# Performance work log

Hardware: AMD Instinct MI355X
Metric: run time of the kernel (lower is better)

The kernel has to match this reference:

```python
import jax, jax.numpy as jnp
import numpy as np

DIM = 1024
HEADS = 16
HEAD_DIM = DIM // HEADS
B, N = 4, 4096


def setup_inputs() -> dict:
    key = jax.random.key(0)
    ks = jax.random.split(key, 10)
    s = 1.0 / np.sqrt(DIM)
    return {
        "x": jax.random.normal(ks[0], (B, N, DIM), dtype=jnp.float32),
        "Wq": jax.random.uniform(ks[1], (DIM, DIM), jnp.float32, -s, s),
        "bq": jax.random.uniform(ks[2], (DIM,), jnp.float32, -s, s),
        "Wk": jax.random.uniform(ks[3], (DIM, DIM), jnp.float32, -s, s),
        "bk": jax.random.uniform(ks[4], (DIM,), jnp.float32, -s, s),
        "Wv": jax.random.uniform(ks[5], (DIM, DIM), jnp.float32, -s, s),
        "bv": jax.random.uniform(ks[6], (DIM,), jnp.float32, -s, s),
        "Wo": jax.random.uniform(ks[7], (DIM, DIM), jnp.float32, -s, s),
        "bo": jax.random.uniform(ks[8], (DIM,), jnp.float32, -s, s),
        "stdp": jnp.ones((HEADS,), dtype=jnp.float32),
    }


def reference(x, Wq, bq, Wk, bk, Wv, bv, Wo, bo, stdp):
    b, n, d = x.shape
    h, dh = HEADS, HEAD_DIM
    # projections (torch Linear: x @ W.T + b)
    def proj(W, bias):
        return (x @ W.T + bias).reshape(b, n, h, dh).transpose(0, 2, 1, 3)  # bhnd
    Q = jax.nn.elu(proj(Wq, bq)) + 1.0
    K = jax.nn.elu(proj(Wk, bk)) + 1.0
    V = proj(Wv, bv)
    stdp_w = jax.nn.sigmoid(stdp).reshape(1, h, 1, 1)
    KV = jnp.einsum('bhnd,bhnv->bhdv', K, V)      # (b,h,dh,dh)
    K_sum = K.sum(axis=2)                          # (b,h,dh)
    numerator = jnp.einsum('bhnd,bhdv->bhnv', Q, KV)
    denominator = jnp.einsum('bhnd,bhd->bhn', Q, K_sum)[..., None] + 1e-6
    attn_out = numerator / denominator * stdp_w    # (b,h,n,dh)
    out = attn_out.transpose(0, 2, 1, 3).reshape(b, n, d)
    out = out @ Wo.T + bo
    return (out, jax.lax.stop_gradient(stdp))
```

## Files before the change

### kernel.cpp

```cpp
#include <hip/hip_runtime.h>
#include <hip/hip_bf16.h>

#define DIMSZ 1024
#define SEQLEN 4096
#define NHEAD 16
#define NX 16777216L
#define NW 1048576L
#define KVSPLITS 8

typedef __attribute__((ext_vector_type(8))) short bf16x8;
typedef __attribute__((ext_vector_type(4))) float f32x4;

__device__ __forceinline__ unsigned short f2bf(float f) {
    union { float f; unsigned int i; } c; c.f = f;
    unsigned int x = c.i;
    unsigned int r = (x + 0x7fffu + ((x >> 16) & 1u)) >> 16;
    return (unsigned short)r;
}

__device__ __forceinline__ unsigned int pk2(float lo, float hi) {
    union { float f; unsigned int i; } a, b; a.f = lo; b.f = hi;
    return __builtin_amdgcn_perm(b.i + 0x8000u, a.i + 0x8000u, 0x07060302u);
}

__device__ __forceinline__ void unp8r(bf16x8 v, float* f) {
    union { bf16x8 s; uint4 w; } u; u.s = v;
    union { unsigned int i; float f; } c;
    c.i = u.w.x << 16;           f[0] = c.f;
    c.i = u.w.x & 0xffff0000u;   f[1] = c.f;
    c.i = u.w.y << 16;           f[2] = c.f;
    c.i = u.w.y & 0xffff0000u;   f[3] = c.f;
    c.i = u.w.z << 16;           f[4] = c.f;
    c.i = u.w.z & 0xffff0000u;   f[5] = c.f;
    c.i = u.w.w << 16;           f[6] = c.f;
    c.i = u.w.w & 0xffff0000u;   f[7] = c.f;
}

__device__ __forceinline__ void async16(const void* g, void* l) {
    __builtin_amdgcn_global_load_lds(
        (const __attribute__((address_space(1))) void*)g,
        (__attribute__((address_space(3))) void*)l,
        16, 0, 0);
}

__global__ __launch_bounds__(256) void cast_pack(
    const float* __restrict__ x, const float* __restrict__ Wq,
    const float* __restrict__ Wk, const float* __restrict__ Wv,
    const float* __restrict__ Wo, const float* __restrict__ stdp,
    unsigned short* __restrict__ xb, unsigned short* __restrict__ Wqkv,
    unsigned short* __restrict__ Wob, float* __restrict__ outTail)
{
    long i4 = ((long)blockIdx.x * 256 + threadIdx.x) * 4;
    const float* src; unsigned short* dst; long off;
    if (i4 < NX)               { src = x;  dst = xb;          off = i4; }
    else if (i4 < NX + NW)     { src = Wq; dst = Wqkv;        off = i4 - NX; }
    else if (i4 < NX + 2*NW)   { src = Wk; dst = Wqkv + NW;   off = i4 - NX - NW; }
    else if (i4 < NX + 3*NW)   { src = Wv; dst = Wqkv + 2*NW; off = i4 - NX - 2*NW; }
    else                       { src = Wo; dst = Wob;         off = i4 - NX - 3*NW; }
    float4 v = *(const float4*)(src + off);
    union { unsigned short u[4]; uint2 p; } o;
    o.u[0] = f2bf(v.x); o.u[1] = f2bf(v.y); o.u[2] = f2bf(v.z); o.u[3] = f2bf(v.w);
    *(uint2*)(dst + off) = o.p;
    if (blockIdx.x == 0 && threadIdx.x < NHEAD) outTail[threadIdx.x] = stdp[threadIdx.x];
}

__global__ __launch_bounds__(512, 2) void qkv_gemm8(
    const unsigned short* __restrict__ A, const unsigned short* __restrict__ W,
    const float* __restrict__ bq, const float* __restrict__ bk,
    const float* __restrict__ bv,
    unsigned short* __restrict__ Qb, unsigned short* __restrict__ Kb,
    unsigned short* __restrict__ Vb)
{
    __shared__ __align__(16) char SM[131072];
    const int t = threadIdx.x;
    const int wave = t >> 6, lane = t & 63;
    const int lr = lane & 15, lq = lane >> 4;
    const int wm = wave >> 2, wn = wave & 3;
    const int m0 = blockIdx.x * 256;
    const int c0 = blockIdx.y * 256;

    const int sc = (((t & 7) ^ ((t >> 3) & 7)) * 8);
    const unsigned short* pA = A + (long)(m0 + (t >> 3)) * DIMSZ + sc;
    const unsigned short* pB = W + (long)(c0 + (t >> 3)) * DIMSZ + sc;
    char* ldsW = SM + wave * 1024;

    const int xo = ((lq ^ (lr & 7)) << 4);
    const char* ABase = SM + wm * 16384 + lr * 128;
    const char* BBase = SM + 32768 + (wn * 64 + lr) * 128;

    f32x4 acc[8][4];
    #pragma unroll
    for (int i = 0; i < 8; ++i)
        #pragma unroll
        for (int j = 0; j < 4; ++j) acc[i][j] = (f32x4){0.f, 0.f, 0.f, 0.f};

#define STAGE(Q, O) do {                                                        \
        if ((Q) < 16) {                                                         \
            const int isB_ = ((O) < 2) ? 1 : 0;                                 \
            const int half_ = isB_ ? (O) : ((O) - 2);                           \
            const unsigned short* s_ = (isB_ ? pB : pA)                         \
                                       + (long)half_ * 131072 + (Q) * 64;       \
            char* d_ = ldsW + (((Q) & 1) << 16) + isB_ * 32768 + half_ * 16384; \
            async16(s_, d_);                                                    \
            async16(s_ + 65536, d_ + 8192);                                     \
        }                                                                       \
    } while (0)

    STAGE(0, 0); STAGE(0, 1); STAGE(0, 2); STAGE(0, 3);
    STAGE(1, 0); STAGE(1, 1); STAGE(1, 2);
    asm volatile("s_waitcnt vmcnt(6)" ::: "memory");
    __builtin_amdgcn_s_barrier();

    for (int kt = 0; kt < 16; ++kt) {
        const int buf = (kt & 1) << 16;
        bf16x8 a0[4][2], a1[4][2], bfr[4][2];

        #pragma unroll
        for (int j = 0; j < 2; ++j) {
            bfr[j][0] = *(const bf16x8*)(BBase + buf + j * 2048 + xo);
            bfr[j][1] = *(const bf16x8*)(BBase + buf + j * 2048 + (xo ^ 64));
        }
        #pragma unroll
        for (int i = 0; i < 4; ++i) {
            a0[i][0] = *(const bf16x8*)(ABase + buf + i * 2048 + xo);
            a0[i][1] = *(const bf16x8*)(ABase + buf + i * 2048 + (xo ^ 64));
        }
        __builtin_amdgcn_sched_barrier(0);
        #pragma unroll
        for (int j = 2; j < 4; ++j) {
            bfr[j][0] = *(const bf16x8*)(BBase + buf + j * 2048 + xo);
            bfr[j][1] = *(const bf16x8*)(BBase + buf + j * 2048 + (xo ^ 64));
        }
        __builtin_amdgcn_sched_barrier(0);
        #pragma unroll
        for (int i = 0; i < 4; ++i) {
            a1[i][0] = *(const bf16x8*)(ABase + buf + (i + 4) * 2048 + xo);
            a1[i][1] = *(const bf16x8*)(ABase + buf + (i + 4) * 2048 + (xo ^ 64));
        }
        __builtin_amdgcn_sched_barrier(0);
        STAGE(kt + 1, 3);

        asm volatile("s_waitcnt lgkmcnt(12)" ::: "memory");
        __builtin_amdgcn_sched_barrier(0);
        __builtin_amdgcn_s_setprio(1);
        #pragma unroll
        for (int s = 0; s < 2; ++s)
            #pragma unroll
            for (int i = 0; i < 4; ++i)
                #pragma unroll
                for (int j = 0; j < 2; ++j)
                    acc[i][j] = __builtin_amdgcn_mfma_f32_16x16x32_bf16(
                        bfr[j][s], a0[i][s], acc[i][j], 0, 0, 0);
        __builtin_amdgcn_s_setprio(0);

        asm volatile("s_waitcnt lgkmcnt(8)" ::: "memory");
        __builtin_amdgcn_sched_barrier(0);
        __builtin_amdgcn_s_setprio(1);
        #pragma unroll
        for (int s = 0; s < 2; ++s)
            #pragma unroll
            for (int i = 0; i < 4; ++i)
                #pragma unroll
                for (int j = 2; j < 4; ++j)
                    acc[i][j] = __builtin_amdgcn_mfma_f32_16x16x32_bf16(
                        bfr[j][s], a0[i][s], acc[i][j], 0, 0, 0);
        __builtin_amdgcn_s_setprio(0);

        asm volatile("s_waitcnt lgkmcnt(0)" ::: "memory");
        __builtin_amdgcn_sched_barrier(0);
        __builtin_amdgcn_s_setprio(1);
        #pragma unroll
        for (int s = 0; s < 2; ++s)
            #pragma unroll
            for (int i = 0; i < 4; ++i)
                #pragma unroll
                for (int j = 0; j < 2; ++j)
                    acc[i + 4][j] = __builtin_amdgcn_mfma_f32_16x16x32_bf16(
                        bfr[j][s], a1[i][s], acc[i + 4][j], 0, 0, 0);
        __builtin_amdgcn_s_setprio(0);

        __builtin_amdgcn_s_barrier();
        STAGE(kt + 2, 0); STAGE(kt + 2, 1); STAGE(kt + 2, 2);

        __builtin_amdgcn_s_setprio(1);
        #pragma unroll
        for (int s = 0; s < 2; ++s)
            #pragma unroll
            for (int i = 0; i < 4; ++i)
                #pragma unroll
                for (int j = 2; j < 4; ++j)
                    acc[i + 4][j] = __builtin_amdgcn_mfma_f32_16x16x32_bf16(
                        bfr[j][s], a1[i][s], acc[i + 4][j], 0, 0, 0);
        __builtin_amdgcn_s_setprio(0);

        if (kt < 14)       asm volatile("s_waitcnt vmcnt(6)" ::: "memory");
        else if (kt == 14) asm volatile("s_waitcnt vmcnt(0)" ::: "memory");
        __builtin_amdgcn_s_barrier();
    }
#undef STAGE

    const int proj = c0 >> 10;
    const float* bias = proj == 0 ? bq : (proj == 1 ? bk : bv);
    const bool qk = proj < 2;
    const int cb = (c0 & 1023) + wn * 64;
    const int q4 = lq * 4;
    #pragma unroll
    for (int j = 0; j < 4; ++j) {
        const float4 b4 = *(const float4*)(bias + cb + 16 * j + q4);
        #pragma unroll
        for (int i = 0; i < 8; ++i) {
            float v0 = acc[i][j][0] + b4.x, v1 = acc[i][j][1] + b4.y;
            float v2 = acc[i][j][2] + b4.z, v3 = acc[i][j][3] + b4.w;
            if (qk) {
                v0 = v0 > 0.f ? v0 + 1.f : __expf(v0);
                v1 = v1 > 0.f ? v1 + 1.f : __expf(v1);
                v2 = v2 > 0.f ? v2 + 1.f : __expf(v2);
                v3 = v3 > 0.f ? v3 + 1.f : __expf(v3);
            }
            const int row = wm * 128 + 16 * i + lr;
            int byte = row * 512 + wn * 128 + j * 32 + q4 * 2;
            byte ^= (row & 7) << 4;
            uint2 pkd; pkd.x = pk2(v0, v1); pkd.y = pk2(v2, v3);
            *(uint2*)(SM + byte) = pkd;
        }
    }
    __syncthreads();
    unsigned short* dstp = proj == 0 ? Qb : (proj == 1 ? Kb : Vb);
    const int colsh = (t & 31) * 8;
    const int h = ((c0 >> 6) + (colsh >> 6)) & 15;
    const int b_ = m0 >> 12;
    unsigned short* dbase = dstp + ((long)(b_ * 16 + h) * SEQLEN) * 64 + (colsh & 63);
    #pragma unroll
    for (int u = 0; u < 16; ++u) {
        const int flat = u * 8192 + t * 16;
        const int row = flat >> 9;
        uint4 val = *(const uint4*)(SM + (flat ^ ((row & 7) << 4)));
        const int n = (m0 + row) & 4095;
        *(uint4*)(dbase + (long)n * 64) = val;
    }
}

__global__ __launch_bounds__(256) void kv_reduce(
    const unsigned short* __restrict__ Kb, const unsigned short* __restrict__ Vb,
    float* __restrict__ KVp, float* __restrict__ Ksump)
{
    __shared__ __align__(16) char LDS[65536];
    int bh = blockIdx.x, split = blockIdx.y, t = threadIdx.x;
    int wave = t >> 6, lane = t & 63, lr = lane & 15, lq = lane >> 4;

    const int nl = t & 127;
    const int dh = (t >> 7) * 32;
    const int vrow = 16 * wave + lr;

    f32x4 acc[4];
    #pragma unroll
    for (int j = 0; j < 4; ++j) acc[j] = (f32x4){0.f, 0.f, 0.f, 0.f};
    float ksp[4] = {0.f, 0.f, 0.f, 0.f};

    for (int half = 0; half < 2; ++half) {
        const unsigned short* Kbase = Kb + ((long)bh * SEQLEN + split * 512 + half * 256) * 64;
        const unsigned short* Vbase = Vb + ((long)bh * SEQLEN + split * 512 + half * 256) * 64;

        union Q2S { uint4 q[4]; unsigned short s[32]; };
        Q2S kq[2], vq[2];
        #pragma unroll
        for (int it = 0; it < 2; ++it) {
            const unsigned short* kp = Kbase + (long)(it * 128 + nl) * 64 + dh;
            const unsigned short* vp = Vbase + (long)(it * 128 + nl) * 64 + dh;
            #pragma unroll
            for (int g = 0; g < 4; ++g) {
                kq[it].q[g] = *(const uint4*)(kp + g * 8);
                vq[it].q[g] = *(const uint4*)(vp + g * 8);
            }
        }
        if (half) __syncthreads();
        #pragma unroll
        for (int it = 0; it < 2; ++it) {
            char* buf = LDS + it * 32768;
            #pragma unroll
            for (int e = 0; e < 32; ++e) {
                const int d = dh + e;
                const int a = d * 256 + ((nl * 2) ^ ((d & 7) << 4));
                *(unsigned short*)(buf + a) = kq[it].s[e];
                *(unsigned short*)(buf + 16384 + a) = vq[it].s[e];
            }
        }
        __syncthreads();

        #pragma unroll
        for (int it = 0; it < 2; ++it) {
            const char* buf = LDS + it * 32768;
            #pragma unroll
            for (int ns = 0; ns < 4; ++ns) {
                const int xoff = (ns * 64 + lq * 16) ^ ((lr & 7) << 4);
                bf16x8 af = *(const bf16x8*)(buf + 16384 + vrow * 256 + xoff);
                bf16x8 bfr[4];
                #pragma unroll
                for (int j = 0; j < 4; ++j)
                    bfr[j] = *(const bf16x8*)(buf + (16 * j + lr) * 256 + xoff);
                if (wave == 0) {
                    #pragma unroll
                    for (int j = 0; j < 4; ++j) {
                        float kf[8]; unp8r(bfr[j], kf);
                        ksp[j] += ((kf[0] + kf[1]) + (kf[2] + kf[3]))
                                + ((kf[4] + kf[5]) + (kf[6] + kf[7]));
                    }
                }
                #pragma unroll
                for (int j = 0; j < 4; ++j)
                    acc[j] = __builtin_amdgcn_mfma_f32_16x16x32_bf16(bfr[j], af, acc[j], 0, 0, 0);
            }
        }
    }

    float* kp = KVp + ((long)split * 64 + bh) * 4096;
    const int q4 = lq * 4;
    #pragma unroll
    for (int j = 0; j < 4; ++j)
        *(f32x4*)(kp + vrow * 64 + 16 * j + q4) = acc[j];

    if (wave == 0) {
        #pragma unroll
        for (int j = 0; j < 4; ++j) {
            float s = ksp[j];
            s += __shfl_xor(s, 16);
            s += __shfl_xor(s, 32);
            if (lane < 16)
                Ksump[((long)split * 64 + bh) * 64 + 16 * j + lr] = s;
        }
    }
}

__global__ __launch_bounds__(256) void kv_final(
    const float* __restrict__ KVp, const float* __restrict__ Ksump,
    unsigned short* __restrict__ KVb, float* __restrict__ Ksum)
{
    int bh = blockIdx.x, t = threadIdx.x;
    float s[16];
    #pragma unroll
    for (int g = 0; g < 16; ++g) s[g] = 0.f;
    for (int sp = 0; sp < KVSPLITS; ++sp) {
        const float* src = KVp + ((long)sp * 64 + bh) * 4096 + t * 16;
        #pragma unroll
        for (int g = 0; g < 4; ++g) {
            float4 v = *(const float4*)(src + g * 4);
            s[g * 4 + 0] += v.x; s[g * 4 + 1] += v.y;
            s[g * 4 + 2] += v.z; s[g * 4 + 3] += v.w;
        }
    }
    uint4 o0, o1;
    o0.x = pk2(s[0], s[1]);  o0.y = pk2(s[2], s[3]);
    o0.z = pk2(s[4], s[5]);  o0.w = pk2(s[6], s[7]);
    o1.x = pk2(s[8], s[9]);  o1.y = pk2(s[10], s[11]);
    o1.z = pk2(s[12], s[13]); o1.w = pk2(s[14], s[15]);
    *(uint4*)(KVb + (long)bh * 4096 + t * 16) = o0;
    *(uint4*)(KVb + (long)bh * 4096 + t * 16 + 8) = o1;
    if (t < 16) {
        float4 a = {0.f, 0.f, 0.f, 0.f};
        for (int p = 0; p < KVSPLITS; p += 4) {
            #pragma unroll
            for (int q = 0; q < 4; ++q) {
                float4 v = *(const float4*)(Ksump + ((long)(p + q) * 64 + bh) * 64 + t * 4);
                a.x += v.x; a.y += v.y; a.z += v.z; a.w += v.w;
            }
        }
        *(float4*)(Ksum + bh * 64 + t * 4) = a;
    }
}

__global__ __launch_bounds__(256) void attn_kernel(
    const unsigned short* __restrict__ Qb, const unsigned short* __restrict__ KVb,
    const float* __restrict__ Ksum, const float* __restrict__ stdp,
    unsigned short* __restrict__ attn)
{
    __shared__ unsigned short Cs[256 * 72];
    int t = threadIdx.x;
    int bh = blockIdx.y;
    int b = bh >> 4, h = bh & 15;

    int wave = t >> 6, lane = t & 63, lr = lane & 15, lk = (lane >> 4) * 8;
    const unsigned short* kvb = KVb + (long)bh * 4096;
    const float* ksb = Ksum + bh * 64;

    bf16x8 bfrh[2][4];
    float ksf[2][8];
    #pragma unroll
    for (int s = 0; s < 2; ++s) {
        #pragma unroll
        for (int j = 0; j < 4; ++j)
            bfrh[s][j] = *(const bf16x8*)(kvb + (16 * j + lr) * 64 + s * 32 + lk);
        float4 ka = *(const float4*)(ksb + s * 32 + lk);
        float4 kb2 = *(const float4*)(ksb + s * 32 + lk + 4);
        ksf[s][0] = ka.x; ksf[s][1] = ka.y; ksf[s][2] = ka.z; ksf[s][3] = ka.w;
        ksf[s][4] = kb2.x; ksf[s][5] = kb2.y; ksf[s][6] = kb2.z; ksf[s][7] = kb2.w;
    }
    float sg = 1.f / (1.f + __expf(-stdp[h]));
    int q4 = (lane >> 4) * 4;

    for (int c = 0; c < 2; ++c) {
        int rc = blockIdx.x * 2 + c;
        int rowbase = rc * 256 + wave * 64;

        f32x4 acc[4][4];
        #pragma unroll
        for (int i = 0; i < 4; ++i)
            #pragma unroll
            for (int j = 0; j < 4; ++j) acc[i][j] = (f32x4){0.f, 0.f, 0.f, 0.f};
        float ds[4] = {0.f, 0.f, 0.f, 0.f};

        #pragma unroll
        for (int s = 0; s < 2; ++s) {
            bf16x8 af[4];
            #pragma unroll
            for (int i = 0; i < 4; ++i)
                af[i] = *(const bf16x8*)(Qb + ((long)bh * SEQLEN + rowbase + 16 * i + lr) * 64 + s * 32 + lk);
            #pragma unroll
            for (int i = 0; i < 4; ++i) {
                float qf[8]; unp8r(af[i], qf);
                #pragma unroll
                for (int e = 0; e < 8; ++e) ds[i] += qf[e] * ksf[s][e];
            }
            #pragma unroll
            for (int i = 0; i < 4; ++i)
                #pragma unroll
                for (int j = 0; j < 4; ++j)
                    acc[i][j] = __builtin_amdgcn_mfma_f32_16x16x32_bf16(bfrh[s][j], af[i], acc[i][j], 0, 0, 0);
        }

        float dinv_i[4];
        #pragma unroll
        for (int i = 0; i < 4; ++i) {
            float d = ds[i];
            d += __shfl_xor(d, 16);
            d += __shfl_xor(d, 32);
            dinv_i[i] = sg / (d + 1e-6f);
        }

        #pragma unroll
        for (int j = 0; j < 4; ++j) {
            int v0c = 16 * j + q4;
            #pragma unroll
            for (int i = 0; i < 4; ++i) {
                int row = wave * 64 + 16 * i + lr;
                float d = dinv_i[i];
                uint2 pkd;
                pkd.x = pk2(acc[i][j][0] * d, acc[i][j][1] * d);
                pkd.y = pk2(acc[i][j][2] * d, acc[i][j][3] * d);
                *(uint2*)(Cs + row * 72 + v0c) = pkd;
            }
        }
        __syncthreads();
        #pragma unroll
        for (int u = 0; u < 8; ++u) {
            int row = u * 32 + (t >> 3);
            int nn = rc * 256 + row;
            long a = ((long)(b * SEQLEN + nn)) * DIMSZ + h * 64 + (t & 7) * 8;
            *(uint4*)(attn + a) = *(const uint4*)(Cs + row * 72 + (t & 7) * 8);
        }
        __syncthreads();
    }
}

__global__ __launch_bounds__(512, 2) void out_gemm8(
    const unsigned short* __restrict__ A, const unsigned short* __restrict__ W,
    const float* __restrict__ bo, float* __restrict__ out)
{
    __shared__ __align__(16) char SM[131072];
    const int t = threadIdx.x;
    const int wave = t >> 6, lane = t & 63;
    const int lr = lane & 15, lq = lane >> 4;
    const int wm = wave >> 2, wn = wave & 3;
    const int m0 = blockIdx.x * 256;
    const int c0 = blockIdx.y * 256;

    const int sc = (((t & 7) ^ ((t >> 3) & 7)) * 8);
    const unsigned short* pA = A + (long)(m0 + (t >> 3)) * DIMSZ + sc;
    const unsigned short* pB = W + (long)(c0 + (t >> 3)) * DIMSZ + sc;
    char* ldsW = SM + wave * 1024;

    const int xo = ((lq ^ (lr & 7)) << 4);
    const char* ABase = SM + wm * 16384 + lr * 128;
    const char* BBase = SM + 32768 + (wn * 64 + lr) * 128;

    f32x4 acc[8][4];
    #pragma unroll
    for (int i = 0; i < 8; ++i)
        #pragma unroll
        for (int j = 0; j < 4; ++j) acc[i][j] = (f32x4){0.f, 0.f, 0.f, 0.f};

#define STAGE(Q, O) do {                                                        \
        if ((Q) < 16) {                                                         \
            const int isB_ = ((O) < 2) ? 1 : 0;                                 \
            const int half_ = isB_ ? (O) : ((O) - 2);                           \
            const unsigned short* s_ = (isB_ ? pB : pA)                         \
                                       + (long)half_ * 131072 + (Q) * 64;       \
            char* d_ = ldsW + (((Q) & 1) << 16) + isB_ * 32768 + half_ * 16384; \
            async16(s_, d_);                                                    \
            async16(s_ + 65536, d_ + 8192);                                     \
        }                                                                       \
    } while (0)

    STAGE(0, 0); STAGE(0, 1); STAGE(0, 2); STAGE(0, 3);
    STAGE(1, 0); STAGE(1, 1); STAGE(1, 2);
    asm volatile("s_waitcnt vmcnt(6)" ::: "memory");
    __builtin_amdgcn_s_barrier();

    for (int kt = 0; kt < 16; ++kt) {
        const int buf = (kt & 1) << 16;
        bf16x8 a0[4][2], a1[4][2], bfr[4][2];

        #pragma unroll
        for (int j = 0; j < 2; ++j) {
            bfr[j][0] = *(const bf16x8*)(BBase + buf + j * 2048 + xo);
            bfr[j][1] = *(const bf16x8*)(BBase + buf + j * 2048 + (xo ^ 64));
        }
        #pragma unroll
        for (int i = 0; i < 4; ++i) {
            a0[i][0] = *(const bf16x8*)(ABase + buf + i * 2048 + xo);
            a0[i][1] = *(const bf16x8*)(ABase + buf + i * 2048 + (xo ^ 64));
        }
        __builtin_amdgcn_sched_barrier(0);
        #pragma unroll
        for (int j = 2; j < 4; ++j) {
            bfr[j][0] = *(const bf16x8*)(BBase + buf + j * 2048 + xo);
            bfr[j][1] = *(const bf16x8*)(BBase + buf + j * 2048 + (xo ^ 64));
        }
        __builtin_amdgcn_sched_barrier(0);
        #pragma unroll
        for (int i = 0; i < 4; ++i) {
            a1[i][0] = *(const bf16x8*)(ABase + buf + (i + 4) * 2048 + xo);
            a1[i][1] = *(const bf16x8*)(ABase + buf + (i + 4) * 2048 + (xo ^ 64));
        }
        __builtin_amdgcn_sched_barrier(0);
        STAGE(kt + 1, 3);

        asm volatile("s_waitcnt lgkmcnt(12)" ::: "memory");
        __builtin_amdgcn_sched_barrier(0);
        __builtin_amdgcn_s_setprio(1);
        #pragma unroll
        for (int s = 0; s < 2; ++s)
            #pragma unroll
            for (int i = 0; i < 4; ++i)
                #pragma unroll
                for (int j = 0; j < 2; ++j)
                    acc[i][j] = __builtin_amdgcn_mfma_f32_16x16x32_bf16(
                        bfr[j][s], a0[i][s], acc[i][j], 0, 0, 0);
        __builtin_amdgcn_s_setprio(0);

        asm volatile("s_waitcnt lgkmcnt(8)" ::: "memory");
        __builtin_amdgcn_sched_barrier(0);
        __builtin_amdgcn_s_setprio(1);
        #pragma unroll
        for (int s = 0; s < 2; ++s)
            #pragma unroll
            for (int i = 0; i < 4; ++i)
                #pragma unroll
                for (int j = 2; j < 4; ++j)
                    acc[i][j] = __builtin_amdgcn_mfma_f32_16x16x32_bf16(
                        bfr[j][s], a0[i][s], acc[i][j], 0, 0, 0);
        __builtin_amdgcn_s_setprio(0);

        asm volatile("s_waitcnt lgkmcnt(0)" ::: "memory");
        __builtin_amdgcn_sched_barrier(0);
        __builtin_amdgcn_s_setprio(1);
        #pragma unroll
        for (int s = 0; s < 2; ++s)
            #pragma unroll
            for (int i = 0; i < 4; ++i)
                #pragma unroll
                for (int j = 0; j < 2; ++j)
                    acc[i + 4][j] = __builtin_amdgcn_mfma_f32_16x16x32_bf16(
                        bfr[j][s], a1[i][s], acc[i + 4][j], 0, 0, 0);
        __builtin_amdgcn_s_setprio(0);

        __builtin_amdgcn_s_barrier();
        STAGE(kt + 2, 0); STAGE(kt + 2, 1); STAGE(kt + 2, 2);

        __builtin_amdgcn_s_setprio(1);
        #pragma unroll
        for (int s = 0; s < 2; ++s)
            #pragma unroll
            for (int i = 0; i < 4; ++i)
                #pragma unroll
                for (int j = 2; j < 4; ++j)
                    acc[i + 4][j] = __builtin_amdgcn_mfma_f32_16x16x32_bf16(
                        bfr[j][s], a1[i][s], acc[i + 4][j], 0, 0, 0);
        __builtin_amdgcn_s_setprio(0);

        if (kt < 14)       asm volatile("s_waitcnt vmcnt(6)" ::: "memory");
        else if (kt == 14) asm volatile("s_waitcnt vmcnt(0)" ::: "memory");
        __builtin_amdgcn_s_barrier();
    }
#undef STAGE

    const int q4 = lq * 4;
    #pragma unroll
    for (int j = 0; j < 4; ++j) {
        const int c = c0 + wn * 64 + 16 * j + q4;
        const float4 b4 = *(const float4*)(bo + c);
        #pragma unroll
        for (int i = 0; i < 8; ++i) {
            const int gm = m0 + wm * 128 + 16 * i + lr;
            float4 v;
            v.x = acc[i][j][0] + b4.x; v.y = acc[i][j][1] + b4.y;
            v.z = acc[i][j][2] + b4.z; v.w = acc[i][j][3] + b4.w;
            *(float4*)(out + (long)gm * DIMSZ + c) = v;
        }
    }
}

extern "C" void kernel_launch(void* const* d_in, const int* in_sizes, int n_in,
                              void* d_out, int out_size, void* d_ws, size_t ws_size,
                              hipStream_t stream) {
    const float* x    = (const float*)d_in[0];
    const float* Wq   = (const float*)d_in[1];
    const float* bq   = (const float*)d_in[2];
    const float* Wk   = (const float*)d_in[3];
    const float* bk   = (const float*)d_in[4];
    const float* Wv   = (const float*)d_in[5];
    const float* bv   = (const float*)d_in[6];
    const float* Wo   = (const float*)d_in[7];
    const float* bo   = (const float*)d_in[8];
    const float* stdp = (const float*)d_in[9];
    float* out = (float*)d_out;

    char* ws = (char*)d_ws;
    unsigned short* xb   = (unsigned short*)(ws);
    float*          KVp  = (float*)(ws);
    unsigned short* attn = (unsigned short*)(ws);
    unsigned short* Wqkv = (unsigned short*)(ws + 33554432L);
    float*          Ksump= (float*)(ws + 33554432L);
    unsigned short* KVb  = (unsigned short*)(ws + 33816576L);
    float*          Ksum = (float*)(ws + 34340864L);
    unsigned short* Wob  = (unsigned short*)(ws + 39845888L);
    unsigned short* Qb   = (unsigned short*)(ws + 41943040L);
    unsigned short* Kb   = (unsigned short*)(ws + 75497472L);
    unsigned short* Vb   = (unsigned short*)(ws + 109051904L);

    cast_pack<<<20480, 256, 0, stream>>>(x, Wq, Wk, Wv, Wo, stdp, xb, Wqkv, Wob,
                                         out + 16777216L);
    qkv_gemm8<<<dim3(64, 12), 512, 0, stream>>>(xb, Wqkv, bq, bk, bv, Qb, Kb, Vb);
    kv_reduce<<<dim3(64, KVSPLITS), 256, 0, stream>>>(Kb, Vb, KVp, Ksump);
    kv_final<<<64, 256, 0, stream>>>(KVp, Ksump, KVb, Ksum);
    attn_kernel<<<dim3(8, 64), 256, 0, stream>>>(Qb, KVb, Ksum, stdp, attn);
    out_gemm8<<<dim3(64, 4), 512, 0, stream>>>(attn, Wob, bo, out);
}
```

Measured before the change: 315.4 us.

## Use 1024-thread blocks in GEMMs with 16 waves sharing each 256x256 tile

Both bf16 GEMM kernels go from 512 threads (8 waves, 128x64 per wave) to 1024 threads (16 waves, 64x64 per wave) on the same 256x256 block tile. Each thread issues half the async global-to-LDS copies, and the K-slice of fragment loads is split into two halves to cut register pressure. The goal is more waves to hide memory latency and fewer accumulators per thread. The cost is one block per CU, since the launch bounds change from (512,2) to (1024,1) with 128KB of LDS per block, plus more barrier participants and less fragment reuse per wave.

```diff
diff --git a/kernel.cpp b/kernel.cpp
--- a/kernel.cpp
+++ b/kernel.cpp
@@ -64,7 +64,7 @@
     if (blockIdx.x == 0 && threadIdx.x < NHEAD) outTail[threadIdx.x] = stdp[threadIdx.x];
 }
 
-__global__ __launch_bounds__(512, 2) void qkv_gemm8(
+__global__ __launch_bounds__(1024, 1) void qkv_gemm8(
     const unsigned short* __restrict__ A, const unsigned short* __restrict__ W,
     const float* __restrict__ bq, const float* __restrict__ bk,
     const float* __restrict__ bv,
@@ -85,12 +85,12 @@
     char* ldsW = SM + wave * 1024;
 
     const int xo = ((lq ^ (lr & 7)) << 4);
-    const char* ABase = SM + wm * 16384 + lr * 128;
+    const char* ABase = SM + wm * 8192 + lr * 128;
     const char* BBase = SM + 32768 + (wn * 64 + lr) * 128;
 
-    f32x4 acc[8][4];
-    #pragma unroll
-    for (int i = 0; i < 8; ++i)
+    f32x4 acc[4][4];
+    #pragma unroll
+    for (int i = 0; i < 4; ++i)
         #pragma unroll
         for (int j = 0; j < 4; ++j) acc[i][j] = (f32x4){0.f, 0.f, 0.f, 0.f};
 
@@ -102,98 +102,87 @@
                                        + (long)half_ * 131072 + (Q) * 64;       \
             char* d_ = ldsW + (((Q) & 1) << 16) + isB_ * 32768 + half_ * 16384; \
             async16(s_, d_);                                                    \
-            async16(s_ + 65536, d_ + 8192);                                     \
         }                                                                       \
     } while (0)
 
     STAGE(0, 0); STAGE(0, 1); STAGE(0, 2); STAGE(0, 3);
     STAGE(1, 0); STAGE(1, 1); STAGE(1, 2);
-    asm volatile("s_waitcnt vmcnt(6)" ::: "memory");
+    asm volatile("s_waitcnt vmcnt(3)" ::: "memory");
     __builtin_amdgcn_s_barrier();
 
     for (int kt = 0; kt < 16; ++kt) {
         const int buf = (kt & 1) << 16;
-        bf16x8 a0[4][2], a1[4][2], bfr[4][2];
-
-        #pragma unroll
-        for (int j = 0; j < 2; ++j) {
-            bfr[j][0] = *(const bf16x8*)(BBase + buf + j * 2048 + xo);
-            bfr[j][1] = *(const bf16x8*)(BBase + buf + j * 2048 + (xo ^ 64));
-        }
-        #pragma unroll
-        for (int i = 0; i < 4; ++i) {
-            a0[i][0] = *(const bf16x8*)(ABase + buf + i * 2048 + xo);
-            a0[i][1] = *(const bf16x8*)(ABase + buf + i * 2048 + (xo ^ 64));
-        }
-        __builtin_amdgcn_sched_barrier(0);
-        #pragma unroll
-        for (int j = 2; j < 4; ++j) {
-            bfr[j][0] = *(const bf16x8*)(BBase + buf + j * 2048 + xo);
-            bfr[j][1] = *(const bf16x8*)(BBase + buf + j * 2048 + (xo ^ 64));
-        }
-        __builtin_amdgcn_sched_barrier(0);
-        #pragma unroll
-        for (int i = 0; i < 4; ++i) {
-            a1[i][0] = *(const bf16x8*)(ABase + buf + (i + 4) * 2048 + xo);
-            a1[i][1] = *(const bf16x8*)(ABase + buf + (i + 4) * 2048 + (xo ^ 64));
-        }
+        bf16x8 a[4], b[4];
+
+        b[0] = *(const bf16x8*)(BBase + buf + 0 * 2048 + xo);
+        b[1] = *(const bf16x8*)(BBase + buf + 1 * 2048 + xo);
+        #pragma unroll
+        for (int i = 0; i < 4; ++i)
+            a[i] = *(const bf16x8*)(ABase + buf + i * 2048 + xo);
+        __builtin_amdgcn_sched_barrier(0);
+        b[2] = *(const bf16x8*)(BBase + buf + 2 * 2048 + xo);
+        b[3] = *(const bf16x8*)(BBase + buf + 3 * 2048 + xo);
         __builtin_amdgcn_sched_barrier(0);
         STAGE(kt + 1, 3);
 
-        asm volatile("s_waitcnt lgkmcnt(12)" ::: "memory");
-        __builtin_amdgcn_sched_barrier(0);
-        __builtin_amdgcn_s_setprio(1);
-        #pragma unroll
-        for (int s = 0; s < 2; ++s)
-            #pragma unroll
-            for (int i = 0; i < 4; ++i)
-                #pragma unroll
-                for (int j = 0; j < 2; ++j)
-                    acc[i][j] = __builtin_amdgcn_mfma_f32_16x16x32_bf16(
-                        bfr[j][s], a0[i][s], acc[i][j], 0, 0, 0);
-        __builtin_amdgcn_s_setprio(0);
-
-        asm volatile("s_waitcnt lgkmcnt(8)" ::: "memory");
-        __builtin_amdgcn_sched_barrier(0);
-        __builtin_amdgcn_s_setprio(1);
-        #pragma unroll
-        for (int s = 0; s < 2; ++s)
-            #pragma unroll
-            for (int i = 0; i < 4; ++i)
-                #pragma unroll
-                for (int j = 2; j < 4; ++j)
-                    acc[i][j] = __builtin_amdgcn_mfma_f32_16x16x32_bf16(
-                        bfr[j][s], a0[i][s], acc[i][j], 0, 0, 0);
+        asm volatile("s_waitcnt lgkmcnt(2)" ::: "memory");
+        __builtin_amdgcn_sched_barrier(0);
+        __builtin_amdgcn_s_setprio(1);
+        #pragma unroll
+        for (int i = 0; i < 4; ++i)
+            #pragma unroll
+            for (int j = 0; j < 2; ++j)
+                acc[i][j] = __builtin_amdgcn_mfma_f32_16x16x32_bf16(
+                    b[j], a[i], acc[i][j], 0, 0, 0);
         __builtin_amdgcn_s_setprio(0);
 
         asm volatile("s_waitcnt lgkmcnt(0)" ::: "memory");
         __builtin_amdgcn_sched_barrier(0);
         __builtin_amdgcn_s_setprio(1);
         #pragma unroll
-        for (int s = 0; s < 2; ++s)
-            #pragma unroll
-            for (int i = 0; i < 4; ++i)
-                #pragma unroll
-                for (int j = 0; j < 2; ++j)
-                    acc[i + 4][j] = __builtin_amdgcn_mfma_f32_16x16x32_bf16(
-                        bfr[j][s], a1[i][s], acc[i + 4][j], 0, 0, 0);
-        __builtin_amdgcn_s_setprio(0);
-
+        for (int i = 0; i < 4; ++i)
+            #pragma unroll
+            for (int j = 2; j < 4; ++j)
+                acc[i][j] = __builtin_amdgcn_mfma_f32_16x16x32_bf16(
+                    b[j], a[i], acc[i][j], 0, 0, 0);
+        __builtin_amdgcn_s_setprio(0);
+
+        b[0] = *(const bf16x8*)(BBase + buf + 0 * 2048 + (xo ^ 64));
+        b[1] = *(const bf16x8*)(BBase + buf + 1 * 2048 + (xo ^ 64));
+        #pragma unroll
+        for (int i = 0; i < 4; ++i)
+            a[i] = *(const bf16x8*)(ABase + buf + i * 2048 + (xo ^ 64));
+        __builtin_amdgcn_sched_barrier(0);
+        b[2] = *(const bf16x8*)(BBase + buf + 2 * 2048 + (xo ^ 64));
+        b[3] = *(const bf16x8*)(BBase + buf + 3 * 2048 + (xo ^ 64));
+        __builtin_amdgcn_sched_barrier(0);
+
+        asm volatile("s_waitcnt lgkmcnt(2)" ::: "memory");
+        __builtin_amdgcn_sched_barrier(0);
+        __builtin_amdgcn_s_setprio(1);
+        #pragma unroll
+        for (int i = 0; i < 4; ++i)
+            #pragma unroll
+            for (int j = 0; j < 2; ++j)
+                acc[i][j] = __builtin_amdgcn_mfma_f32_16x16x32_bf16(
+                    b[j], a[i], acc[i][j], 0, 0, 0);
+        __builtin_amdgcn_s_setprio(0);
+
+        asm volatile("s_waitcnt lgkmcnt(0)" ::: "memory");
+        __builtin_amdgcn_sched_barrier(0);
         __builtin_amdgcn_s_barrier();
         STAGE(kt + 2, 0); STAGE(kt + 2, 1); STAGE(kt + 2, 2);
 
         __builtin_amdgcn_s_setprio(1);
         #pragma unroll
-        for (int s = 0; s < 2; ++s)
-            #pragma unroll
-            for (int i = 0; i < 4; ++i)
-                #pragma unroll
-                for (int j = 2; j < 4; ++j)
-                    acc[i + 4][j] = __builtin_amdgcn_mfma_f32_16x16x32_bf16(
-                        bfr[j][s], a1[i][s], acc[i + 4][j], 0, 0, 0);
-        __builtin_amdgcn_s_setprio(0);
-
-        if (kt < 14)       asm volatile("s_waitcnt vmcnt(6)" ::: "memory");
+        for (int i = 0; i < 4; ++i)
+            #pragma unroll
+            for (int j = 2; j < 4; ++j)
+                acc[i][j] = __builtin_amdgcn_mfma_f32_16x16x32_bf16(
+                    b[j], a[i], acc[i][j], 0, 0, 0);
+        __builtin_amdgcn_s_setprio(0);
+
+        if (kt < 14)       asm volatile("s_waitcnt vmcnt(3)" ::: "memory");
         else if (kt == 14) asm volatile("s_waitcnt vmcnt(0)" ::: "memory");
         __builtin_amdgcn_s_barrier();
     }
@@ -208,7 +197,7 @@
     for (int j = 0; j < 4; ++j) {
         const float4 b4 = *(const float4*)(bias + cb + 16 * j + q4);
         #pragma unroll
-        for (int i = 0; i < 8; ++i) {
+        for (int i = 0; i < 4; ++i) {
             float v0 = acc[i][j][0] + b4.x, v1 = acc[i][j][1] + b4.y;
             float v2 = acc[i][j][2] + b4.z, v3 = acc[i][j][3] + b4.w;
             if (qk) {
@@ -217,7 +206,7 @@
                 v2 = v2 > 0.f ? v2 + 1.f : __expf(v2);
                 v3 = v3 > 0.f ? v3 + 1.f : __expf(v3);
             }
-            const int row = wm * 128 + 16 * i + lr;
+            const int row = wm * 64 + 16 * i + lr;
             int byte = row * 512 + wn * 128 + j * 32 + q4 * 2;
             byte ^= (row & 7) << 4;
             uint2 pkd; pkd.x = pk2(v0, v1); pkd.y = pk2(v2, v3);
@@ -231,8 +220,8 @@
     const int b_ = m0 >> 12;
     unsigned short* dbase = dstp + ((long)(b_ * 16 + h) * SEQLEN) * 64 + (colsh & 63);
     #pragma unroll
-    for (int u = 0; u < 16; ++u) {
-        const int flat = u * 8192 + t * 16;
+    for (int u = 0; u < 8; ++u) {
+        const int flat = u * 16384 + t * 16;
         const int row = flat >> 9;
         uint4 val = *(const uint4*)(SM + (flat ^ ((row & 7) << 4)));
         const int n = (m0 + row) & 4095;
@@ -461,7 +450,7 @@
     }
 }
 
-__global__ __launch_bounds__(512, 2) void out_gemm8(
+__global__ __launch_bounds__(1024, 1) void out_gemm8(
     const unsigned short* __restrict__ A, const unsigned short* __restrict__ W,
     const float* __restrict__ bo, float* __restrict__ out)
 {
@@ -479,12 +468,12 @@
     char* ldsW = SM + wave * 1024;
 
     const int xo = ((lq ^ (lr & 7)) << 4);
-    const char* ABase = SM + wm * 16384 + lr * 128;
+    const char* ABase = SM + wm * 8192 + lr * 128;
     const char* BBase = SM + 32768 + (wn * 64 + lr) * 128;
 
-    f32x4 acc[8][4];
-    #pragma unroll
-    for (int i = 0; i < 8; ++i)
+    f32x4 acc[4][4];
+    #pragma unroll
+    for (int i = 0; i < 4; ++i)
         #pragma unroll
         for (int j = 0; j < 4; ++j) acc[i][j] = (f32x4){0.f, 0.f, 0.f, 0.f};
 
@@ -496,98 +485,87 @@
                                        + (long)half_ * 131072 + (Q) * 64;       \
             char* d_ = ldsW + (((Q) & 1) << 16) + isB_ * 32768 + half_ * 16384; \
             async16(s_, d_);                                                    \
-            async16(s_ + 65536, d_ + 8192);                                     \
         }                                                                       \
     } while (0)
 
     STAGE(0, 0); STAGE(0, 1); STAGE(0, 2); STAGE(0, 3);
     STAGE(1, 0); STAGE(1, 1); STAGE(1, 2);
-    asm volatile("s_waitcnt vmcnt(6)" ::: "memory");
+    asm volatile("s_waitcnt vmcnt(3)" ::: "memory");
     __builtin_amdgcn_s_barrier();
 
     for (int kt = 0; kt < 16; ++kt) {
         const int buf = (kt & 1) << 16;
-        bf16x8 a0[4][2], a1[4][2], bfr[4][2];
-
-        #pragma unroll
-        for (int j = 0; j < 2; ++j) {
-            bfr[j][0] = *(const bf16x8*)(BBase + buf + j * 2048 + xo);
-            bfr[j][1] = *(const bf16x8*)(BBase + buf + j * 2048 + (xo ^ 64));
-        }
-        #pragma unroll
-        for (int i = 0; i < 4; ++i) {
-            a0[i][0] = *(const bf16x8*)(ABase + buf + i * 2048 + xo);
-            a0[i][1] = *(const bf16x8*)(ABase + buf + i * 2048 + (xo ^ 64));
-        }
-        __builtin_amdgcn_sched_barrier(0);
-        #pragma unroll
-        for (int j = 2; j < 4; ++j) {
-            bfr[j][0] = *(const bf16x8*)(BBase + buf + j * 2048 + xo);
-            bfr[j][1] = *(const bf16x8*)(BBase + buf + j * 2048 + (xo ^ 64));
-        }
-        __builtin_amdgcn_sched_barrier(0);
-        #pragma unroll
-        for (int i = 0; i < 4; ++i) {
-            a1[i][0] = *(const bf16x8*)(ABase + buf + (i + 4) * 2048 + xo);
-            a1[i][1] = *(const bf16x8*)(ABase + buf + (i + 4) * 2048 + (xo ^ 64));
-        }
+        bf16x8 a[4], b[4];
+
+        b[0] = *(const bf16x8*)(BBase + buf + 0 * 2048 + xo);
+        b[1] = *(const bf16x8*)(BBase + buf + 1 * 2048 + xo);
+        #pragma unroll
+        for (int i = 0; i < 4; ++i)
+            a[i] = *(const bf16x8*)(ABase + buf + i * 2048 + xo);
+        __builtin_amdgcn_sched_barrier(0);
+        b[2] = *(const bf16x8*)(BBase + buf + 2 * 2048 + xo);
+        b[3] = *(const bf16x8*)(BBase + buf + 3 * 2048 + xo);
         __builtin_amdgcn_sched_barrier(0);
         STAGE(kt + 1, 3);
 
-        asm volatile("s_waitcnt lgkmcnt(12)" ::: "memory");
-        __builtin_amdgcn_sched_barrier(0);
-        __builtin_amdgcn_s_setprio(1);
-        #pragma unroll
-        for (int s = 0; s < 2; ++s)
-            #pragma unroll
-            for (int i = 0; i < 4; ++i)
-                #pragma unroll
-                for (int j = 0; j < 2; ++j)
-                    acc[i][j] = __builtin_amdgcn_mfma_f32_16x16x32_bf16(
-                        bfr[j][s], a0[i][s], acc[i][j], 0, 0, 0);
-        __builtin_amdgcn_s_setprio(0);
-
-        asm volatile("s_waitcnt lgkmcnt(8)" ::: "memory");
-        __builtin_amdgcn_sched_barrier(0);
-        __builtin_amdgcn_s_setprio(1);
-        #pragma unroll
-        for (int s = 0; s < 2; ++s)
-            #pragma unroll
-            for (int i = 0; i < 4; ++i)
-                #pragma unroll
-                for (int j = 2; j < 4; ++j)
-                    acc[i][j] = __builtin_amdgcn_mfma_f32_16x16x32_bf16(
-                        bfr[j][s], a0[i][s], acc[i][j], 0, 0, 0);
+        asm volatile("s_waitcnt lgkmcnt(2)" ::: "memory");
+        __builtin_amdgcn_sched_barrier(0);
+        __builtin_amdgcn_s_setprio(1);
+        #pragma unroll
+        for (int i = 0; i < 4; ++i)
+            #pragma unroll
+            for (int j = 0; j < 2; ++j)
+                acc[i][j] = __builtin_amdgcn_mfma_f32_16x16x32_bf16(
+                    b[j], a[i], acc[i][j], 0, 0, 0);
         __builtin_amdgcn_s_setprio(0);
 
         asm volatile("s_waitcnt lgkmcnt(0)" ::: "memory");
         __builtin_amdgcn_sched_barrier(0);
         __builtin_amdgcn_s_setprio(1);
         #pragma unroll
-        for (int s = 0; s < 2; ++s)
-            #pragma unroll
-            for (int i = 0; i < 4; ++i)
-                #pragma unroll
-                for (int j = 0; j < 2; ++j)
-                    acc[i + 4][j] = __builtin_amdgcn_mfma_f32_16x16x32_bf16(
-                        bfr[j][s], a1[i][s], acc[i + 4][j], 0, 0, 0);
-        __builtin_amdgcn_s_setprio(0);
-
+        for (int i = 0; i < 4; ++i)
+            #pragma unroll
+            for (int j = 2; j < 4; ++j)
+                acc[i][j] = __builtin_amdgcn_mfma_f32_16x16x32_bf16(
+                    b[j], a[i], acc[i][j], 0, 0, 0);
+        __builtin_amdgcn_s_setprio(0);
+
+        b[0] = *(const bf16x8*)(BBase + buf + 0 * 2048 + (xo ^ 64));
+        b[1] = *(const bf16x8*)(BBase + buf + 1 * 2048 + (xo ^ 64));
+        #pragma unroll
+        for (int i = 0; i < 4; ++i)
+            a[i] = *(const bf16x8*)(ABase + buf + i * 2048 + (xo ^ 64));
+        __builtin_amdgcn_sched_barrier(0);
+        b[2] = *(const bf16x8*)(BBase + buf + 2 * 2048 + (xo ^ 64));
+        b[3] = *(const bf16x8*)(BBase + buf + 3 * 2048 + (xo ^ 64));
+        __builtin_amdgcn_sched_barrier(0);
+
+        asm volatile("s_waitcnt lgkmcnt(2)" ::: "memory");
+        __builtin_amdgcn_sched_barrier(0);
+        __builtin_amdgcn_s_setprio(1);
+        #pragma unroll
+        for (int i = 0; i < 4; ++i)
+            #pragma unroll
+            for (int j = 0; j < 2; ++j)
+                acc[i][j] = __builtin_amdgcn_mfma_f32_16x16x32_bf16(
+                    b[j], a[i], acc[i][j], 0, 0, 0);
+        __builtin_amdgcn_s_setprio(0);
+
+        asm volatile("s_waitcnt lgkmcnt(0)" ::: "memory");
+        __builtin_amdgcn_sched_barrier(0);
         __builtin_amdgcn_s_barrier();
         STAGE(kt + 2, 0); STAGE(kt + 2, 1); STAGE(kt + 2, 2);
 
         __builtin_amdgcn_s_setprio(1);
         #pragma unroll
-        for (int s = 0; s < 2; ++s)
-            #pragma unroll
-            for (int i = 0; i < 4; ++i)
-                #pragma unroll
-                for (int j = 2; j < 4; ++j)
-                    acc[i + 4][j] = __builtin_amdgcn_mfma_f32_16x16x32_bf16(
-                        bfr[j][s], a1[i][s], acc[i + 4][j], 0, 0, 0);
-        __builtin_amdgcn_s_setprio(0);
-
-        if (kt < 14)       asm volatile("s_waitcnt vmcnt(6)" ::: "memory");
+        for (int i = 0; i < 4; ++i)
+            #pragma unroll
+            for (int j = 2; j < 4; ++j)
+                acc[i][j] = __builtin_amdgcn_mfma_f32_16x16x32_bf16(
+                    b[j], a[i], acc[i][j], 0, 0, 0);
+        __builtin_amdgcn_s_setprio(0);
+
+        if (kt < 14)       asm volatile("s_waitcnt vmcnt(3)" ::: "memory");
         else if (kt == 14) asm volatile("s_waitcnt vmcnt(0)" ::: "memory");
         __builtin_amdgcn_s_barrier();
     }
@@ -599,8 +577,8 @@
         const int c = c0 + wn * 64 + 16 * j + q4;
         const float4 b4 = *(const float4*)(bo + c);
         #pragma unroll
-        for (int i = 0; i < 8; ++i) {
-            const int gm = m0 + wm * 128 + 16 * i + lr;
+        for (int i = 0; i < 4; ++i) {
+            const int gm = m0 + wm * 64 + 16 * i + lr;
             float4 v;
             v.x = acc[i][j][0] + b4.x; v.y = acc[i][j][1] + b4.y;
             v.z = acc[i][j][2] + b4.z; v.w = acc[i][j][3] + b4.w;
@@ -639,9 +617,9 @@
 
     cast_pack<<<20480, 256, 0, stream>>>(x, Wq, Wk, Wv, Wo, stdp, xb, Wqkv, Wob,
                                          out + 16777216L);
-    qkv_gemm8<<<dim3(64, 12), 512, 0, stream>>>(xb, Wqkv, bq, bk, bv, Qb, Kb, Vb);
+    qkv_gemm8<<<dim3(64, 12), 1024, 0, stream>>>(xb, Wqkv, bq, bk, bv, Qb, Kb, Vb);
     kv_reduce<<<dim3(64, KVSPLITS), 256, 0, stream>>>(Kb, Vb, KVp, Ksump);
     kv_final<<<64, 256, 0, stream>>>(KVp, Ksump, KVb, Ksum);
     attn_kernel<<<dim3(8, 64), 256, 0, stream>>>(Qb, KVb, Ksum, stdp, attn);
-    out_gemm8<<<dim3(64, 4), 512, 0, stream>>>(attn, Wob, bo, out);
-}
+    out_gemm8<<<dim3(64, 4), 1024, 0, stream>>>(attn, Wob, bo, out);
+}
```

After: 312.2 us. No clear change (-1.0%).
